# Optimization experiments

Measured on AMD Instinct MI355X. Metric: run time of the kernel, lower is better.

## Reference

```python
import jax, jax.numpy as jnp
import numpy as np

D_MODEL = 512


def setup_inputs() -> dict:
    key = jax.random.key(0)
    ks = jax.random.split(key, 9)
    d = D_MODEL
    s = 1.0 / np.sqrt(d)
    return {
        "x": jax.random.normal(ks[0], (4, 2048, d), dtype=jnp.float32),
        "Wq": jax.random.normal(ks[1], (d, d), dtype=jnp.float32) * s,
        "bq": jax.random.normal(ks[2], (d,), dtype=jnp.float32) * 0.02,
        "Wk": jax.random.normal(ks[3], (d, d), dtype=jnp.float32) * s,
        "bk": jax.random.normal(ks[4], (d,), dtype=jnp.float32) * 0.02,
        "Wv": jax.random.normal(ks[5], (d, d), dtype=jnp.float32) * s,
        "bv": jax.random.normal(ks[6], (d,), dtype=jnp.float32) * 0.02,
        "Wo": jax.random.normal(ks[7], (d, d), dtype=jnp.float32) * s,
        "bo": jax.random.normal(ks[8], (d,), dtype=jnp.float32) * 0.02,
    }


def reference(x, Wq, bq, Wk, bk, Wv, bv, Wo, bo):
    # NOTE: this "MultiHeadedAttention" never splits heads in its forward;
    # Q/K/V are full d_model width. Dropout is treated as eval-mode identity.
    q = jnp.einsum("bnc,dc->bnd", x, Wq) + bq  # torch Linear: x @ W.T + b
    k = jnp.einsum("bnc,dc->bnd", x, Wk) + bk
    v = jnp.einsum("bnc,dc->bnd", x, Wv) + bv
    scale = 1.0 / jnp.sqrt(jnp.asarray(q.shape[-1], q.dtype))
    scores = jnp.einsum("bnd,bmd->bnm", q, k) * scale  # [B, N, N]
    p_attn = jax.nn.softmax(scores, axis=-1)
    att = jnp.einsum("bnm,bmd->bnd", p_attn, v)
    return jnp.einsum("bnd,od->bno", att, Wo) + bo
```

## Files before the change

kernel.cpp:

```cpp
#include <hip/hip_runtime.h>
#include <hip/hip_bf16.h>

#define D_MODEL 512
#define BATCH 4
#define SEQ 2048
#define ROWS (BATCH*SEQ)

typedef unsigned short u16;
typedef short bf16x8 __attribute__((ext_vector_type(8)));
typedef float f32x4 __attribute__((ext_vector_type(4)));

__device__ __forceinline__ float bf2f(u16 u) {
    union { unsigned int i; float f; } v;
    v.i = ((unsigned int)u) << 16;
    return v.f;
}
__device__ __forceinline__ u16 f2bf(float f) {
    union { float f; unsigned int i; } v;
    v.f = f;
    unsigned int x = v.i;
    unsigned int r = (x >> 16) & 1u;
    x += 0x7fffu + r;
    return (u16)(x >> 16);
}

template<int N> __device__ __forceinline__ void waitv() {
    static_assert(N==0 || N==3 || N==4 || N==5 || N==8, "unsupported vmcnt");
    if constexpr (N == 0) asm volatile("s_waitcnt vmcnt(0)" ::: "memory");
    if constexpr (N == 3) asm volatile("s_waitcnt vmcnt(3)" ::: "memory");
    if constexpr (N == 4) asm volatile("s_waitcnt vmcnt(4)" ::: "memory");
    if constexpr (N == 5) asm volatile("s_waitcnt vmcnt(5)" ::: "memory");
    if constexpr (N == 8) asm volatile("s_waitcnt vmcnt(8)" ::: "memory");
}

__global__ __launch_bounds__(256)
void prep_kernel(const float* __restrict__ x,
                 const float* __restrict__ Wq, const float* __restrict__ Wk,
                 const float* __restrict__ Wv, const float* __restrict__ Wo,
                 const float* __restrict__ bq, const float* __restrict__ bk,
                 const float* __restrict__ bv,
                 u16* __restrict__ xh,
                 u16* __restrict__ whh, u16* __restrict__ woh,
                 float* __restrict__ bqkv)
{
    const int blk = blockIdx.x;
    const int tid = threadIdx.x;
    const int WE = 262144;
    if (blk >= 5120) {
        int i = (blk - 5120) * 256 + tid;
        if (i < 1536)
            bqkv[i] = (i < 512) ? bq[i] : (i < 1024) ? bk[i - 512] : bv[i - 1024];
        return;
    }
    const float* src; u16 *dh; int i;
    if (blk < 4096) {
        src = x; dh = xh;
        i = (blk * 256 + tid) * 4;
    } else {
        int w = (blk - 4096) >> 8;
        src = (w == 0) ? Wq : (w == 1) ? Wk : (w == 2) ? Wv : Wo;
        dh  = (w < 3) ? whh + w * WE : woh;
        i = (((blk - 4096) & 255) * 256 + tid) * 4;
    }
    float4 v = *(const float4*)(src + i);
    u16 hh[4] = { f2bf(v.x), f2bf(v.y), f2bf(v.z), f2bf(v.w) };
    *(ushort4*)(dh + i) = make_ushort4(hh[0], hh[1], hh[2], hh[3]);
}

#define GEMM_PROLOG_ID                                                         \
    const int tid  = threadIdx.x;                                              \
    const int lane = tid & 63;                                                 \
    const int wave = tid >> 6;                                                 \
    const int wr = wave >> 1, wc = wave & 1;                                   \
    const int gx = gridDim.x, gy = gridDim.y;                                  \
    int nwg = gx * gy * gridDim.z;                                             \
    int wg  = blockIdx.x + gx * (blockIdx.y + gy * blockIdx.z);                \
    int id  = (wg & 7) * (nwg >> 3) + (wg >> 3);                               \
    int bx, by, bz;

#define GEMM_PROLOG_BODY                                                       \
    const long aBase = (long)bz * aStride + (long)(bx * 128) * lda;            \
    const long bBase = (long)bz * bStride + (long)(by * BN) * ldb;             \
    const u16* csrc[CPW];                                                      \
    unsigned cdst[CPW];                                                        \
    _Pragma("unroll")                                                          \
    for (int i = 0; i < CPW; ++i) {                                            \
        int c = wave + i * 4;                                                  \
        const u16* sb; int ld, lofs, row;                                      \
        if (c < AT * ACH) {                                                    \
            int t = c >> 3;                                                    \
            row = (c & 7) * 16;                                                \
            sb = (t == 0 ? Ah : Al) + aBase;                                   \
            ld = lda; lofs = t * TILE_A;                                       \
        } else {                                                               \
            int cb = c - AT * ACH;                                             \
            int t = cb / BCH;                                                  \
            row = (cb % BCH) * 16;                                             \
            sb = (t == 0 ? Bh : Bl) + bBase;                                   \
            ld = ldb; lofs = AT * TILE_A + t * TILE_B;                         \
        }                                                                      \
        csrc[i] = sb + (long)(row + (lane >> 2)) * ld + (lane & 3) * 8;        \
        cdst[i] = lofs + row * 32;                                             \
    }                                                                          \
    f32x4 acc[4][NF] = {};                                                     \
    const int frow = lane & 15;                                                \
    const int kofs = (lane >> 4) * 8;

#define GEMM_CONSTS                                                            \
    constexpr int BN     = 32 * NF;                                            \
    constexpr int TILE_A = 128 * 32;                                           \
    constexpr int TILE_B = BN * 32;                                            \
    constexpr int ACH    = 8;                                                  \
    constexpr int BCH    = BN / 16;                                            \
    constexpr int NCH    = AT*ACH + BT*BCH;                                    \
    constexpr int CPW    = NCH / 4;                                            \
    constexpr int BUFSZ  = AT*TILE_A + BT*TILE_B;

#define GEMM_COMPUTE(bb_)                                                      \
    {                                                                          \
        const int bb = (bb_);                                                  \
        bf16x8 aH[4], aL[4], bH[NF], bL[NF];                                   \
        _Pragma("unroll")                                                      \
        for (int m = 0; m < 4; ++m) {                                          \
            int rA = wr*64 + m*16 + frow;                                      \
            aH[m] = *(const bf16x8*)&lds[bb + rA*32 + kofs];                   \
            if constexpr (AT == 2)                                             \
                aL[m] = *(const bf16x8*)&lds[bb + TILE_A + rA*32 + kofs];      \
        }                                                                      \
        _Pragma("unroll")                                                      \
        for (int n = 0; n < NF; ++n) {                                         \
            int rB = wc*(NF*16) + n*16 + frow;                                 \
            bH[n] = *(const bf16x8*)&lds[bb + AT*TILE_A + rB*32 + kofs];       \
            if constexpr (BT == 2)                                             \
                bL[n] = *(const bf16x8*)&lds[bb + AT*TILE_A + TILE_B + rB*32 + kofs]; \
        }                                                                      \
        _Pragma("unroll")                                                      \
        for (int m = 0; m < 4; ++m)                                            \
            _Pragma("unroll")                                                  \
            for (int n = 0; n < NF; ++n) {                                     \
                acc[m][n] = __builtin_amdgcn_mfma_f32_16x16x32_bf16(aH[m], bH[n], acc[m][n], 0, 0, 0); \
                if constexpr (BT == 2)                                         \
                    acc[m][n] = __builtin_amdgcn_mfma_f32_16x16x32_bf16(aH[m], bL[n], acc[m][n], 0, 0, 0); \
                if constexpr (AT == 2)                                         \
                    acc[m][n] = __builtin_amdgcn_mfma_f32_16x16x32_bf16(aL[m], bH[n], acc[m][n], 0, 0, 0); \
            }                                                                  \
    }

#define GEMM_EPILOG_STAGED                                                     \
    {                                                                          \
    const int rr = (lane >> 4) * 4;                                            \
    __syncthreads();                                                           \
    if (emode == 0) {                                                          \
        float* ldsF = (float*)lds;                                             \
        _Pragma("unroll")                                                      \
        for (int n = 0; n < NF; ++n) {                                         \
            int c = wc*(NF*16) + n*16 + frow;                                  \
            float bv_ = ebias ? ebias[by*BN + c] : 0.0f;                       \
            _Pragma("unroll")                                                  \
            for (int m = 0; m < 4; ++m)                                        \
                _Pragma("unroll")                                              \
                for (int j = 0; j < 4; ++j)                                    \
                    ldsF[(wr*64 + m*16 + rr + j)*(BN+4) + c] = acc[m][n][j]*scale + bv_; \
        }                                                                      \
        __syncthreads();                                                       \
        for (int idx = tid; idx < 128*(BN/4); idx += 256) {                    \
            int row = idx / (BN/4), c4 = (idx % (BN/4)) * 4;                   \
            *(float4*)&outF[(long)bz*cStride + (long)(bx*128+row)*ldc + by*BN + c4] = \
                *(float4*)&ldsF[row*(BN+4) + c4];                              \
        }                                                                      \
    } else if (emode == 1) {                                                   \
        u16* ldsH = (u16*)lds;                                                 \
        u16* ldsL = (u16*)lds + 128*(BN+12);                                   \
        _Pragma("unroll")                                                      \
        for (int n = 0; n < NF; ++n) {                                         \
            int c = wc*(NF*16) + n*16 + frow;                                  \
            float bv_ = ebias ? ebias[by*BN + c] : 0.0f;                       \
            _Pragma("unroll")                                                  \
            for (int m = 0; m < 4; ++m)                                        \
                _Pragma("unroll")                                              \
                for (int j = 0; j < 4; ++j) {                                  \
                    int r = wr*64 + m*16 + rr + j;                             \
                    float val = acc[m][n][j]*scale + bv_;                      \
                    u16 h = f2bf(val);                                         \
                    ldsH[r*(BN+12) + c] = h;                                   \
                    if (eoutL) ldsL[r*(BN+12) + c] = f2bf(val - bf2f(h));      \
                }                                                              \
        }                                                                      \
        __syncthreads();                                                       \
        for (int idx = tid; idx < 128*(BN/8); idx += 256) {                    \
            int row = idx / (BN/8), c8 = (idx % (BN/8)) * 8;                   \
            long o = (long)bz*cStride + (long)(bx*128+row)*ldc + by*BN + c8;   \
            *(bf16x8*)&eoutH[o] = *(bf16x8*)&ldsH[row*(BN+12) + c8];           \
            if (eoutL) *(bf16x8*)&eoutL[o] = *(bf16x8*)&ldsL[row*(BN+12) + c8]; \
        }                                                                      \
    } else {                                                                   \
        u16* ldsT = (u16*)lds;                 \
        _Pragma("unroll")                                                      \
        for (int n = 0; n < NF; ++n) {                                         \
            int c = wc*(NF*16) + n*16 + frow;                                  \
            float bv_ = ebias ? ebias[by*BN + c] : 0.0f;                       \
            _Pragma("unroll")                                                  \
            for (int m = 0; m < 4; ++m)                                        \
                _Pragma("unroll")                                              \
                for (int j = 0; j < 4; ++j)                                    \
                    ldsT[c*136 + (wr*64 + m*16 + rr + j)] = f2bf(acc[m][n][j]*scale + bv_); \
        }                                                                      \
        __syncthreads();                                                       \
        int b = bx >> 4, mrowBase = (bx & 15) * 128;                           \
        for (int idx = tid; idx < BN*16; idx += 256) {                         \
            int crow = idx >> 4, r8 = (idx & 15) * 8;                          \
            *(bf16x8*)&eoutH[(long)b*1048576 + (long)(by*BN + crow)*2048 + mrowBase + r8] = \
                *(bf16x8*)&ldsT[crow*136 + r8];                                \
        }                                                                      \
    }                                                                          \
    }

template<int NF, int AT, int BT>
__global__ __launch_bounds__(256)
void gemm2(const u16* __restrict__ Ah, const u16* __restrict__ Al,
           const u16* __restrict__ Bh, const u16* __restrict__ Bl,
           const float* __restrict__ bias,
           float* __restrict__ outF, u16* __restrict__ outH, u16* __restrict__ outL,
           int K, int lda, int ldb, int ldc,
           long aStride, long bStride, long cStride,
           float scale, int mode)
{
    GEMM_CONSTS
    GEMM_PROLOG_ID
    bx = id % gx;
    by = (id / gx) % gy;
    bz = id / (gx * gy);
    GEMM_PROLOG_BODY
    constexpr int EPI1 = 2 * 128*(BN+12);
    constexpr int EPI0 = 256*(BN+4);
    constexpr int L1   = (2*BUFSZ > EPI1) ? 2*BUFSZ : EPI1;
    constexpr int LDSN = (L1 > EPI0) ? L1 : EPI0;
    __shared__ u16 lds[LDSN];
    auto stage = [&](int buf, int k0) {
        #pragma unroll
        for (int i = 0; i < CPW; ++i)
            __builtin_amdgcn_global_load_lds(
                (const __attribute__((address_space(1))) unsigned int*)(csrc[i] + k0),
                (__attribute__((address_space(3))) unsigned int*)(&lds[buf * BUFSZ + cdst[i]]),
                16, 0, 0);
    };
    const int nt = K >> 5;
    stage(0, 0);
    __syncthreads();
    int cur = 0;
    for (int t = 0; t < nt; ++t) {
        if (t + 1 < nt) stage(cur ^ 1, (t + 1) << 5);
        GEMM_COMPUTE(cur * BUFSZ)
        __syncthreads();
        cur ^= 1;
    }
    int emode = mode; const float* ebias = bias; u16* eoutH = outH; u16* eoutL = outL;
    GEMM_EPILOG_STAGED
}

template<int NF, int AT, int BT, int DEC = 0, int ELO = 1>
__global__ __launch_bounds__(256)
void gemm3(const u16* __restrict__ Ah, const u16* __restrict__ Al,
           const u16* __restrict__ Bh, const u16* __restrict__ Bl,
           const float* __restrict__ bias,
           float* __restrict__ outF, u16* __restrict__ outH, u16* __restrict__ outL,
           u16* __restrict__ outQ, u16* __restrict__ outK, u16* __restrict__ outV,
           int K, int lda, int ldb, int ldc,
           long aStride, long bStride, long cStride,
           float scale, int mode)
{
    GEMM_CONSTS
    GEMM_PROLOG_ID
    if constexpr (DEC == 1) {
        constexpr int NBY = 512 / BN;
        constexpr int INN = 3 * NBY;
        int inner = id % INN;
        by = inner % NBY;
        bz = inner / NBY;
        bx = id / INN;
    } else {
        bx = id % gx;
        by = (id / gx) % gy;
        bz = id / (gx * gy);
    }
    GEMM_PROLOG_BODY
    constexpr int EPI1 = (1 + ELO) * 128*(BN+12);
    constexpr int EPI2 = BN * 136;
    constexpr int EPIM = (EPI1 > EPI2) ? EPI1 : EPI2;
    constexpr int LDSN = (3*BUFSZ > EPIM) ? 3*BUFSZ : EPIM;
    __shared__ u16 lds[LDSN];
    auto stage = [&](int buf, int k0) {
        #pragma unroll
        for (int i = 0; i < CPW; ++i)
            __builtin_amdgcn_global_load_lds(
                (const __attribute__((address_space(1))) unsigned int*)(csrc[i] + k0),
                (__attribute__((address_space(3))) unsigned int*)(&lds[buf * BUFSZ + cdst[i]]),
                16, 0, 0);
    };
    const int nt = K >> 5;
    stage(0, 0);
    stage(1, 32);
    for (int t = 0; t < nt; ++t) {
        if (t + 1 < nt) waitv<CPW>();
        else            waitv<0>();
        __builtin_amdgcn_s_barrier();
        __builtin_amdgcn_sched_barrier(0);
        if (t + 2 < nt) stage((t + 2) % 3, (t + 2) << 5);
        GEMM_COMPUTE((t % 3) * BUFSZ)
    }
    int emode = mode; const float* ebias = bias; u16* eoutH = outH; u16* eoutL = outL;
    if (mode == 3) {
        emode = (bz == 2) ? 2 : 1;
        ebias = bias + bz * 512;
        eoutH = (bz == 0) ? outQ : (bz == 1) ? outK : outV;
        eoutL = nullptr;
    }
    GEMM_EPILOG_STAGED
}

__global__ __launch_bounds__(1024, 4)
void gemm256w(const u16* __restrict__ A, const u16* __restrict__ B,
              u16* __restrict__ outH,
              int K, int lda, int ldb, int ldc,
              long aStride, long bStride, long cStride, float scale)
{
    __shared__ u16 lds[2 * 32768];
    const int tid  = threadIdx.x;
    const int lane = tid & 63;
    const int wave = tid >> 6;
    const int wr = wave >> 2, wc = wave & 3;

    const int gx = gridDim.x, gy = gridDim.y;
    int nwg = gx * gy * gridDim.z;
    int wg  = blockIdx.x + gx * (blockIdx.y + gy * blockIdx.z);
    int id  = (wg & 7) * (nwg >> 3) + (wg >> 3);
    const int bx = id % gx;
    const int by = (id / gx) % gy;
    const int bz = id / (gx * gy);

    const long aBase = (long)bz * aStride + (long)(bx * 256) * lda;
    const long bBase = (long)bz * bStride + (long)(by * 256) * ldb;

    const int sw     = wave & 7;
    const bool isB   = wave >= 8;
    const int srow   = lane >> 3;
    const int schunk = (lane & 7) ^ (srow & 7);
    const u16* src_[4];
    unsigned  dst_[4];
    #pragma unroll
    for (int i = 0; i < 4; ++i) {
        int rb = sw * 8 + i * 64;
        src_[i] = (isB ? B + bBase : A + aBase)
                + (long)(rb + srow) * (isB ? ldb : lda) + schunk * 8;
        dst_[i] = (isB ? 16384 : 0) + rb * 64;
    }
    auto stage = [&](int buf, int k0) {
        #pragma unroll
        for (int i = 0; i < 4; ++i)
            __builtin_amdgcn_global_load_lds(
                (const __attribute__((address_space(1))) unsigned int*)(src_[i] + k0),
                (__attribute__((address_space(3))) unsigned int*)(&lds[buf * 32768 + dst_[i]]),
                16, 0, 0);
    };

    f32x4 acc[4][4] = {};
    const int frow = lane & 15;
    const int kq   = lane >> 4;
    const int fswz = frow & 7;

    const int nt = K >> 6;
    stage(0, 0);
    stage(1, 64);
    for (int t = 0; t < nt; ++t) {
        if (t + 1 < nt) waitv<4>(); else waitv<0>();
        __builtin_amdgcn_s_barrier();
        __builtin_amdgcn_sched_barrier(0);
        const int bb = (t & 1) * 32768;
        #pragma unroll
        for (int kh = 0; kh < 2; ++kh) {
            const int ch = ((kh << 2) + kq) ^ fswz;
            bf16x8 aH[4], bH[4];
            #pragma unroll
            for (int m = 0; m < 4; ++m) {
                int rA = wr*64 + m*16 + frow;
                aH[m] = *(const bf16x8*)&lds[bb + rA*64 + ch*8];
            }
            #pragma unroll
            for (int n = 0; n < 4; ++n) {
                int rB = wc*64 + n*16 + frow;
                bH[n] = *(const bf16x8*)&lds[bb + 16384 + rB*64 + ch*8];
            }
            #pragma unroll
            for (int m = 0; m < 4; ++m)
                #pragma unroll
                for (int n = 0; n < 4; ++n)
                    acc[m][n] = __builtin_amdgcn_mfma_f32_16x16x32_bf16(aH[m], bH[n], acc[m][n], 0, 0, 0);
        }
        __builtin_amdgcn_s_barrier();
        __builtin_amdgcn_sched_barrier(0);
        if (t + 2 < nt) stage(t & 1, (t + 2) << 6);
    }

    const int rr = (lane >> 4) * 4;
    #pragma unroll
    for (int h = 0; h < 2; ++h) {
        __syncthreads();
        if ((wr >> 1) == h) {
            #pragma unroll
            for (int n = 0; n < 4; ++n) {
                int c = wc*64 + n*16 + frow;
                #pragma unroll
                for (int m = 0; m < 4; ++m)
                    #pragma unroll
                    for (int j = 0; j < 4; ++j)
                        lds[((wr & 1)*64 + m*16 + rr + j)*264 + c] = f2bf(acc[m][n][j] * scale);
            }
        }
        __syncthreads();
        for (int idx = tid; idx < 128*32; idx += 1024) {
            int row = idx >> 5, c8 = (idx & 31) * 8;
            *(bf16x8*)&outH[(long)bz*cStride + (long)(bx*256 + h*128 + row)*ldc + by*256 + c8] =
                *(bf16x8*)&lds[row*264 + c8];
        }
    }
}

__global__ __launch_bounds__(256)
void softmax_kernel(u16* __restrict__ sh)
{
    const long base = (long)blockIdx.x * 2048;
    const int tid = threadIdx.x;
    const int lane = tid & 63, wave = tid >> 6;
    u16* hp = sh + base + tid * 8;
    bf16x8 hv = *(const bf16x8*)hp;
    float s[8];
    #pragma unroll
    for (int j = 0; j < 8; ++j) s[j] = bf2f((u16)hv[j]);

    float mx = s[0];
    #pragma unroll
    for (int j = 1; j < 8; ++j) mx = fmaxf(mx, s[j]);
    #pragma unroll
    for (int off = 32; off >= 1; off >>= 1) mx = fmaxf(mx, __shfl_xor(mx, off));
    __shared__ float red[8];
    if (lane == 0) red[wave] = mx;
    __syncthreads();
    mx = fmaxf(fmaxf(red[0], red[1]), fmaxf(red[2], red[3]));

    float e[8], sum = 0.f;
    #pragma unroll
    for (int j = 0; j < 8; ++j) { e[j] = __expf(s[j] - mx); sum += e[j]; }
    #pragma unroll
    for (int off = 32; off >= 1; off >>= 1) sum += __shfl_xor(sum, off);
    if (lane == 0) red[4 + wave] = sum;
    __syncthreads();
    sum = red[4] + red[5] + red[6] + red[7];
    float inv = 1.0f / sum;

    bf16x8 ho;
    #pragma unroll
    for (int j = 0; j < 8; ++j) ho[j] = (short)f2bf(e[j] * inv);
    *(bf16x8*)hp = ho;
}

extern "C" void kernel_launch(void* const* d_in, const int* in_sizes, int n_in,
                              void* d_out, int out_size, void* d_ws, size_t ws_size,
                              hipStream_t stream)
{
    const float* x  = (const float*)d_in[0];
    const float* Wq = (const float*)d_in[1];
    const float* bq = (const float*)d_in[2];
    const float* Wk = (const float*)d_in[3];
    const float* bk = (const float*)d_in[4];
    const float* Wv = (const float*)d_in[5];
    const float* bv = (const float*)d_in[6];
    const float* Wo = (const float*)d_in[7];
    const float* bo = (const float*)d_in[8];

    char* p = (char*)d_ws;
    auto alloc = [&](size_t bytes) { char* r = p; p += (bytes + 255) & ~(size_t)255; return r; };

    const size_t XE = (size_t)ROWS * D_MODEL;
    const size_t WE = (size_t)D_MODEL * D_MODEL;
    const size_t SE = (size_t)BATCH * SEQ * SEQ;

    u16* xh   = (u16*)alloc(XE * 2);
    u16* xl   = (u16*)alloc(XE * 2);
    u16* whh  = (u16*)alloc(3 * WE * 2);
    u16* woh  = (u16*)alloc(WE * 2);
    float* bqkv = (float*)alloc(1536 * 4);
    u16* qh   = (u16*)alloc(XE * 2);
    u16* kh   = (u16*)alloc(XE * 2);
    u16* vTh  = (u16*)alloc(XE * 2);
    u16* sh   = (u16*)alloc(SE * 2);
    u16* ath = xh;
    u16* atl = xl;

    prep_kernel<<<5126, 256, 0, stream>>>(x, Wq, Wk, Wv, Wo, bq, bk, bv,
                                          xh, whh, woh, bqkv);

    gemm3<4,1,1,1,0><<<dim3(768, 1, 1), 256, 0, stream>>>(xh, nullptr, whh, nullptr, bqkv,
        nullptr, nullptr, nullptr, qh, kh, vTh,
        512, 512, 512, 512, 0, (long)WE, 0, 1.0f, 3);

    gemm256w<<<dim3(8, 8, 4), 1024, 0, stream>>>(qh, kh, sh,
        512, 512, 512, 2048,
        (long)SEQ * 512, (long)SEQ * 512, (long)SEQ * SEQ,
        0.044194173824159216f);

    softmax_kernel<<<ROWS, 256, 0, stream>>>(sh);

    gemm3<2,1,1,0,1><<<dim3(16, 8, 4), 256, 0, stream>>>(sh, nullptr, vTh, nullptr, nullptr,
        nullptr, ath, atl, nullptr, nullptr, nullptr,
        2048, 2048, 2048, 512,
        (long)SEQ * SEQ, (long)512 * SEQ, (long)SEQ * 512,
        1.0f, 1);

    gemm2<2,2,1><<<dim3(64, 8, 1), 256, 0, stream>>>(ath, atl, woh, nullptr, bo,
        (float*)d_out, nullptr, nullptr, 512, 512, 512, 512,
        0, 0, 0, 1.0f, 0);
}
```

Baseline: 126.6 us.

## Add dedicated 128x128-tile 16-wave kernel for P·V GEMM

Replaces the generic gemm3 launch for the attention-times-V product with a new pv16 kernel. Each 1024-thread workgroup computes a 128x128 output tile using bf16 MFMA, with a triple-buffered LDS pipeline fed by global_load_lds (half the waves load P, half load V). The grid is swizzled across XCDs, and the epilogue writes hi/lo bf16 split outputs through LDS. The goal is better reuse and load/compute overlap for the K=2048 reduction, at the cost of fewer workgroups (256) and high per-block thread counts.

```diff
diff --git a/kernel.cpp b/kernel.cpp
--- a/kernel.cpp
+++ b/kernel.cpp
@@ -25,8 +25,9 @@
 }
 
 template<int N> __device__ __forceinline__ void waitv() {
-    static_assert(N==0 || N==3 || N==4 || N==5 || N==8, "unsupported vmcnt");
+    static_assert(N==0 || N==1 || N==3 || N==4 || N==5 || N==8, "unsupported vmcnt");
     if constexpr (N == 0) asm volatile("s_waitcnt vmcnt(0)" ::: "memory");
+    if constexpr (N == 1) asm volatile("s_waitcnt vmcnt(1)" ::: "memory");
     if constexpr (N == 3) asm volatile("s_waitcnt vmcnt(3)" ::: "memory");
     if constexpr (N == 4) asm volatile("s_waitcnt vmcnt(4)" ::: "memory");
     if constexpr (N == 5) asm volatile("s_waitcnt vmcnt(5)" ::: "memory");
@@ -318,6 +319,102 @@
     GEMM_EPILOG_STAGED
 }
 
+__global__ __launch_bounds__(1024)
+void pv16(const u16* __restrict__ A, const u16* __restrict__ B,
+          u16* __restrict__ outH, u16* __restrict__ outL,
+          int K, int lda, int ldb, int ldc,
+          long aStride, long bStride, long cStride, float scale)
+{
+    constexpr int BUFSZ = 8192;
+    __shared__ u16 lds[3 * BUFSZ];
+    const int tid  = threadIdx.x;
+    const int lane = tid & 63;
+    const int wave = tid >> 6;
+    const int wr = wave >> 2, wc = wave & 3;
+
+    int nwg = gridDim.x;
+    int wg  = blockIdx.x;
+    int id  = (wg & 7) * (nwg >> 3) + (wg >> 3);
+    const int by = id & 3;
+    const int bz = (id >> 2) & 3;
+    const int bx = id >> 4;
+
+    const long aBase = (long)bz * aStride + (long)(bx * 128) * lda;
+    const long bBase = (long)bz * bStride + (long)(by * 128) * ldb;
+
+    const bool isB = wave >= 8;
+    const int  cw  = wave & 7;
+    const u16* csrc = (isB ? B + bBase : A + aBase)
+                    + (long)(cw * 16 + (lane >> 2)) * (isB ? ldb : lda)
+                    + (lane & 3) * 8;
+    const unsigned cdst = (isB ? 4096 : 0) + cw * 512;
+
+    auto stage = [&](int buf, int k0) {
+        __builtin_amdgcn_global_load_lds(
+            (const __attribute__((address_space(1))) unsigned int*)(csrc + k0),
+            (__attribute__((address_space(3))) unsigned int*)(&lds[buf * BUFSZ + cdst]),
+            16, 0, 0);
+    };
+
+    f32x4 acc[2][2] = {};
+    const int frow = lane & 15;
+    const int kofs = (lane >> 4) * 8;
+
+    const int nt = K >> 5;
+    stage(0, 0);
+    stage(1, 32);
+    for (int t = 0; t < nt; ++t) {
+        if (t + 1 < nt) waitv<1>();
+        else            waitv<0>();
+        __builtin_amdgcn_s_barrier();
+        __builtin_amdgcn_sched_barrier(0);
+        if (t + 2 < nt) stage((t + 2) % 3, (t + 2) << 5);
+        const int bb = (t % 3) * BUFSZ;
+        bf16x8 aH[2], bH[2];
+        #pragma unroll
+        for (int m = 0; m < 2; ++m) {
+            int rA = wr*32 + m*16 + frow;
+            aH[m] = *(const bf16x8*)&lds[bb + rA*32 + kofs];
+        }
+        #pragma unroll
+        for (int n = 0; n < 2; ++n) {
+            int rB = wc*32 + n*16 + frow;
+            bH[n] = *(const bf16x8*)&lds[bb + 4096 + rB*32 + kofs];
+        }
+        #pragma unroll
+        for (int m = 0; m < 2; ++m)
+            #pragma unroll
+            for (int n = 0; n < 2; ++n)
+                acc[m][n] = __builtin_amdgcn_mfma_f32_16x16x32_bf16(aH[m], bH[n], acc[m][n], 0, 0, 0);
+    }
+
+    const int rr = (lane >> 4) * 4;
+    #pragma unroll
+    for (int part = 0; part < 2; ++part) {
+        u16* dstG = part ? outL : outH;
+        __syncthreads();
+        #pragma unroll
+        for (int n = 0; n < 2; ++n) {
+            int c = wc*32 + n*16 + frow;
+            #pragma unroll
+            for (int m = 0; m < 2; ++m)
+                #pragma unroll
+                for (int j = 0; j < 4; ++j) {
+                    int r = wr*32 + m*16 + rr + j;
+                    float val = acc[m][n][j] * scale;
+                    u16 h = f2bf(val);
+                    lds[r*140 + c] = part ? f2bf(val - bf2f(h)) : h;
+                }
+        }
+        __syncthreads();
+        for (int idx = tid; idx < 128*16; idx += 1024) {
+            int row = idx >> 4, c8 = (idx & 15) * 8;
+            *(bf16x8*)&dstG[(long)bz*cStride + (long)(bx*128+row)*ldc + by*128 + c8] =
+                *(bf16x8*)&lds[row*140 + c8];
+        }
+    }
+}
+
 __global__ __launch_bounds__(1024, 4)
 void gemm256w(const u16* __restrict__ A, const u16* __restrict__ B,
               u16* __restrict__ outH,
@@ -510,11 +607,9 @@
 
     softmax_kernel<<<ROWS, 256, 0, stream>>>(sh);
 
-    gemm3<2,1,1,0,1><<<dim3(16, 8, 4), 256, 0, stream>>>(sh, nullptr, vTh, nullptr, nullptr,
-        nullptr, ath, atl, nullptr, nullptr, nullptr,
+    pv16<<<dim3(256, 1, 1), 1024, 0, stream>>>(sh, vTh, ath, atl,
         2048, 2048, 2048, 512,
-        (long)SEQ * SEQ, (long)512 * SEQ, (long)SEQ * 512,
-        1.0f, 1);
+        (long)SEQ * SEQ, (long)512 * SEQ, (long)SEQ * 512, 1.0f);
 
     gemm2<2,2,1><<<dim3(64, 8, 1), 256, 0, stream>>>(ath, atl, woh, nullptr, bo,
         (float*)d_out, nullptr, nullptr, 512, 512, 512, 512,
```

Measured after the change: 126.3 us. Within noise of the previous version (-0.3%).
